# Optimization experiments

Hardware: AMD Instinct MI355X
Metric: run time of the kernel (lower is better)

## Reference

```python
import jax, jax.numpy as jnp
import numpy as np

B, D, T = 8, 1024, 512
HID, NH, NL = 256, 4, 2
OUT = HID // NH  # 64 per-head dim
ALPHA = 0.2      # leaky relu slope
EPS = 1e-5       # layernorm eps


def setup_inputs() -> dict:
    key = jax.random.key(0)
    ks = jax.random.split(key, 10)
    X_obs = jax.random.normal(ks[0], (B, D, T), dtype=jnp.float32)
    mask = (jax.random.uniform(ks[1], (B, D, T)) < 0.8).astype(jnp.float32)
    W_in = jax.random.normal(ks[2], (2 * T, HID), dtype=jnp.float32) * (1.0 / np.sqrt(2 * T))
    b_in = jnp.zeros((HID,), dtype=jnp.float32)
    gat_W = jax.random.normal(ks[3], (NL, NH, HID, OUT), dtype=jnp.float32) * (1.0 / np.sqrt(HID))
    gat_a = jax.random.normal(ks[4], (NL, NH, 2 * OUT), dtype=jnp.float32) * 0.1
    ln_g = jnp.ones((NL, HID), dtype=jnp.float32)
    ln_b = jnp.zeros((NL, HID), dtype=jnp.float32)
    W_out = jax.random.normal(ks[5], (HID, T), dtype=jnp.float32) * (1.0 / np.sqrt(HID))
    b_out = jnp.zeros((T,), dtype=jnp.float32)
    return dict(X_obs=X_obs, mask=mask, W_in=W_in, b_in=b_in, gat_W=gat_W,
                gat_a=gat_a, ln_g=ln_g, ln_b=ln_b, W_out=W_out, b_out=b_out)


def _layer_norm(x, g, b):
    mu = jnp.mean(x, axis=-1, keepdims=True)
    var = jnp.mean((x - mu) ** 2, axis=-1, keepdims=True)
    return (x - mu) * jax.lax.rsqrt(var + EPS) * g + b


def _gat_forward(X_obs, mask, W_in, b_in, gat_W, gat_a, ln_g, ln_b, W_out, b_out):
    # mean-impute per (d, t) position across batch
    obs_sum = jnp.sum(X_obs * mask, axis=0, keepdims=True)
    obs_cnt = jnp.sum(mask, axis=0, keepdims=True)
    pos_mean = obs_sum / (obs_cnt + 1e-10)
    X_mean = X_obs * mask + (1.0 - mask) * pos_mean

    x = jnp.concatenate([X_mean, mask], axis=-1)       # (B, D, 2T)
    h = x @ W_in + b_in                                 # (B, N, HID)

    for l in range(NL):
        Wl = gat_W[l]                                   # (H, HID, OUT)
        a_left = gat_a[l, :, :OUT]                      # (H, OUT)
        a_right = gat_a[l, :, OUT:]                     # (H, OUT)
        hW = jnp.einsum('bnd,hde->bhne', h, Wl)         # (B, H, N, OUT)
        # e_ij = leakyrelu(a_left . h_i + a_right . h_j) -- avoids O(N^2 * 2d) concat
        s_l = jnp.einsum('bhne,he->bhn', hW, a_left)
        s_r = jnp.einsum('bhne,he->bhn', hW, a_right)
        e = jax.nn.leaky_relu(s_l[..., :, None] + s_r[..., None, :], ALPHA)  # (B,H,N,N)
        attn = jax.nn.softmax(e, axis=-1)
        head_out = jnp.einsum('bhnm,bhme->bhne', attn, hW)                   # (B,H,N,OUT)
        h_new = jnp.transpose(head_out, (0, 2, 1, 3)).reshape(h.shape[0], h.shape[1], HID)
        h = _layer_norm(h + h_new, ln_g[l], ln_b[l])

    return h @ W_out + b_out                            # (B, D, T)


def reference(X_obs, mask, W_in, b_in, gat_W, gat_a, ln_g, ln_b, W_out, b_out):
    return _gat_forward(X_obs, mask, W_in, b_in, gat_W, gat_a, ln_g, ln_b, W_out, b_out)
```

## Files before the change

kernel.cpp:

```cpp
#include <hip/hip_runtime.h>
#include <hip/hip_bf16.h>

constexpr int B_   = 8;
constexpr int D_   = 1024;
constexpr int T_   = 512;
constexpr int HID_ = 256;
constexpr int NH_  = 4;
constexpr int NL_  = 2;
constexpr float ALPHA_ = 0.2f;
constexpr float EPS_   = 1e-5f;
constexpr int OUT_ = 64;
constexpr int M_ = B_ * D_;
constexpr int DT_ = D_ * T_;
constexpr int KIN_ = 2 * T_;
constexpr int CKS_ = 132;

typedef __attribute__((ext_vector_type(8))) short short8;
typedef __attribute__((ext_vector_type(4))) float floatx4;

__device__ __forceinline__ unsigned short f2bf(float f) {
    unsigned int u = __float_as_uint(f);
    unsigned int r = u + 0x7fffu + ((u >> 16) & 1u);
    return (unsigned short)(r >> 16);
}
__device__ __forceinline__ float bf2f(unsigned short u) {
    return __uint_as_float(((unsigned int)u) << 16);
}
__device__ __forceinline__ unsigned int kenc(float f) {
    unsigned int u = __float_as_uint(f);
    return (u & 0x80000000u) ? ~u : (u | 0x80000000u);
}
__device__ __forceinline__ float kdec(unsigned int k) {
    unsigned int u = (k & 0x80000000u) ? (k ^ 0x80000000u) : ~k;
    return __uint_as_float(u);
}

__global__ __launch_bounds__(256) void prep_k(const float* __restrict__ X,
                                              const float* __restrict__ Mk,
                                              const float* __restrict__ W_in,
                                              const float* __restrict__ gatW,
                                              const float* __restrict__ W_out,
                                              unsigned short* __restrict__ Ain,
                                              unsigned short* __restrict__ Wt_in,
                                              unsigned short* __restrict__ Wcat,
                                              unsigned short* __restrict__ WtO,
                                              unsigned int* __restrict__ rmaxkey) {
    int bx = blockIdx.x;
    if (bx < 512) {
        int idx4 = (bx * 256 + threadIdx.x) * 4;
        int t = idx4 & (T_ - 1);
        int d = idx4 >> 9;
        float4 x[B_], m[B_];
        float4 s = {0, 0, 0, 0}, c = {0, 0, 0, 0};
#pragma unroll
        for (int b = 0; b < B_; b++) {
            x[b] = *(const float4*)&X[(size_t)b * DT_ + idx4];
            m[b] = *(const float4*)&Mk[(size_t)b * DT_ + idx4];
            s.x += x[b].x * m[b].x; s.y += x[b].y * m[b].y;
            s.z += x[b].z * m[b].z; s.w += x[b].w * m[b].w;
            c.x += m[b].x; c.y += m[b].y; c.z += m[b].z; c.w += m[b].w;
        }
        float4 pm;
        pm.x = s.x / (c.x + 1e-10f); pm.y = s.y / (c.y + 1e-10f);
        pm.z = s.z / (c.z + 1e-10f); pm.w = s.w / (c.w + 1e-10f);
#pragma unroll
        for (int b = 0; b < B_; b++) {
            size_t row = (size_t)b * D_ + d;
            ushort4 xm, mk;
            xm.x = f2bf(x[b].x * m[b].x + (1.f - m[b].x) * pm.x);
            xm.y = f2bf(x[b].y * m[b].y + (1.f - m[b].y) * pm.y);
            xm.z = f2bf(x[b].z * m[b].z + (1.f - m[b].z) * pm.z);
            xm.w = f2bf(x[b].w * m[b].w + (1.f - m[b].w) * pm.w);
            mk.x = f2bf(m[b].x); mk.y = f2bf(m[b].y);
            mk.z = f2bf(m[b].z); mk.w = f2bf(m[b].w);
            *(ushort4*)&Ain[row * KIN_ + t]      = xm;
            *(ushort4*)&Ain[row * KIN_ + T_ + t] = mk;
        }
    } else {
        int idx = (bx - 512) * 256 + threadIdx.x;
        if (idx < 64) rmaxkey[idx] = 0u;
        if (idx < 262144) {
            int n = idx >> 10, k = idx & 1023;
            Wt_in[idx] = f2bf(W_in[(size_t)k * HID_ + n]);
        } else if (idx < 393216) {
            int j = idx - 262144;
            int l = j >> 16, n = (j >> 8) & 255, k = j & 255;
            int h = n >> 6, e = n & 63;
            Wcat[j] = f2bf(gatW[(((size_t)(l * NH_ + h) * HID_) + k) * OUT_ + e]);
        } else {
            int j = idx - 393216;
            int n = j >> 8, k = j & 255;
            WtO[j] = f2bf(W_out[(size_t)k * T_ + n]);
        }
    }
}

template <int MODE>
__global__ __launch_bounds__(256) void gemm_bf16_k(
        const unsigned short* __restrict__ A,
        const unsigned short* __restrict__ Bt,
        const float* __restrict__ bias,
        float* __restrict__ C,
        unsigned short* __restrict__ Cb,
        const float* __restrict__ ga,
        float* __restrict__ s_l,
        float* __restrict__ s_r,
        unsigned int* __restrict__ rmaxkey,
        int Nsz, int Ksz) {
    __shared__ __align__(16) unsigned short As[2][64 * 72];
    __shared__ __align__(16) unsigned short Bs[2][64 * 72];
    int tid = threadIdx.x;
    int wave = tid >> 6, lane = tid & 63;
    int q = lane >> 4, r16 = lane & 15;
    int rowbase = blockIdx.y * 64;
    int colbase = blockIdx.x * 64;

    int srow = tid >> 3, sk = (tid & 7) * 8;
    const unsigned short* Ap0 = A + (size_t)(rowbase + srow) * Ksz + sk;
    const unsigned short* Ap1 = A + (size_t)(rowbase + srow + 32) * Ksz + sk;
    const unsigned short* Bp0 = Bt + (size_t)(colbase + srow) * Ksz + sk;
    const unsigned short* Bp1 = Bt + (size_t)(colbase + srow + 32) * Ksz + sk;
    int la0 = srow * 72 + sk, la1 = (srow + 32) * 72 + sk;

    floatx4 acc[4];
#pragma unroll
    for (int i = 0; i < 4; i++) acc[i] = (floatx4)0.f;

    uint4 pa0 = *(const uint4*)Ap0, pa1 = *(const uint4*)Ap1;
    uint4 pb0 = *(const uint4*)Bp0, pb1 = *(const uint4*)Bp1;
    *(uint4*)&As[0][la0] = pa0;
    *(uint4*)&As[0][la1] = pa1;
    *(uint4*)&Bs[0][la0] = pb0;
    *(uint4*)&Bs[0][la1] = pb1;

    int nk = Ksz >> 6;
    for (int it = 0; it < nk; it++) {
        int cur = it & 1;
        __syncthreads();
        if (it + 1 < nk) {
            int kt = (it + 1) << 6;
            pa0 = *(const uint4*)(Ap0 + kt);
            pa1 = *(const uint4*)(Ap1 + kt);
            pb0 = *(const uint4*)(Bp0 + kt);
            pb1 = *(const uint4*)(Bp1 + kt);
        }
#pragma unroll
        for (int t = 0; t < 2; t++) {
            short8 a = *(const short8*)&As[cur][(wave * 16 + r16) * 72 + t * 32 + q * 8];
#pragma unroll
            for (int ni = 0; ni < 4; ni++) {
                short8 b = *(const short8*)&Bs[cur][(ni * 16 + r16) * 72 + t * 32 + q * 8];
                acc[ni] = __builtin_amdgcn_mfma_f32_16x16x32_bf16(a, b, acc[ni], 0, 0, 0);
            }
        }
        if (it + 1 < nk) {
            int nxt = cur ^ 1;
            *(uint4*)&As[nxt][la0] = pa0;
            *(uint4*)&As[nxt][la1] = pa1;
            *(uint4*)&Bs[nxt][la0] = pb0;
            *(uint4*)&Bs[nxt][la1] = pb1;
        }
    }
    if constexpr (MODE == 2) {
        int bhh = ((rowbase >> 10) << 2) + blockIdx.x;
        int nb = (rowbase & (D_ - 1)) + wave * 16;
#pragma unroll
        for (int ni = 0; ni < 4; ni++) {
            int e = ni * 16 + r16;
#pragma unroll
            for (int rr = 0; rr < 4; rr++) {
                int m = nb + q * 4 + rr;
                Cb[((size_t)bhh << 16) + ((size_t)m << 6) + e] = f2bf(acc[ni][rr]);
            }
        }
        const float* gab = ga + blockIdx.x * 2 * OUT_;
        float al4[4], ar4[4];
#pragma unroll
        for (int ni = 0; ni < 4; ni++) {
            al4[ni] = gab[ni * 16 + r16];
            ar4[ni] = gab[OUT_ + ni * 16 + r16];
        }
        float slv[4], srv[4];
#pragma unroll
        for (int rr = 0; rr < 4; rr++) {
            float s1 = 0.f, s2 = 0.f;
#pragma unroll
            for (int ni = 0; ni < 4; ni++) {
                s1 += acc[ni][rr] * al4[ni];
                s2 += acc[ni][rr] * ar4[ni];
            }
            slv[rr] = s1;
            srv[rr] = s2;
        }
#pragma unroll
        for (int off = 1; off < 16; off <<= 1) {
#pragma unroll
            for (int rr = 0; rr < 4; rr++) {
                slv[rr] += __shfl_xor(slv[rr], off, 64);
                srv[rr] += __shfl_xor(srv[rr], off, 64);
            }
        }
        {
            int rsel = r16 & 3;
            float sv = (rsel == 0) ? slv[0] : (rsel == 1) ? slv[1] : (rsel == 2) ? slv[2] : slv[3];
            float rv = (rsel == 0) ? srv[0] : (rsel == 1) ? srv[1] : (rsel == 2) ? srv[2] : srv[3];
            int n = nb + q * 4 + rsel;
            if (r16 < 4)                 s_l[bhh * D_ + n] = sv;
            else if (r16 >= 8 && r16 < 12) s_r[bhh * D_ + n] = rv;
        }
        float mx = fmaxf(fmaxf(srv[0], srv[1]), fmaxf(srv[2], srv[3]));
        mx = fmaxf(mx, __shfl_xor(mx, 16, 64));
        mx = fmaxf(mx, __shfl_xor(mx, 32, 64));
        if (lane == 0) atomicMax(&rmaxkey[bhh], kenc(mx));
    } else {
#pragma unroll
        for (int rr = 0; rr < 4; rr++) {
            int row = rowbase + wave * 16 + q * 4 + rr;
#pragma unroll
            for (int ni = 0; ni < 4; ni++) {
                int col = colbase + ni * 16 + r16;
                float v = acc[ni][rr] + (bias ? bias[col] : 0.f);
                C[(size_t)row * Nsz + col] = v;
                if constexpr (MODE == 1) Cb[(size_t)row * Nsz + col] = f2bf(v);
            }
        }
    }
}

__global__ __launch_bounds__(1024) void rank_k(
        const float* __restrict__ sr_g,
        const unsigned int* __restrict__ rmaxkey,
        float* __restrict__ srt,
        int* __restrict__ sig,
        float* __restrict__ wm) {
    __shared__ float skey[1024];
    __shared__ short part[16][64];
    int bh = blockIdx.x, seg = blockIdx.y;
    int tid = threadIdx.x;
    skey[tid] = sr_g[bh * D_ + tid];
    __syncthreads();
    int lane = tid & 63, wv = tid >> 6;
    int el = seg * 64 + lane;
    float k = skey[el];
    int m0 = wv * 64;
    int cnt = 0;
#pragma unroll 4
    for (int m = m0; m < m0 + 64; ++m) {
        float km = skey[m];
        cnt += (km < k) || (km == k && m < el);
    }
    part[wv][lane] = (short)cnt;
    __syncthreads();
    if (tid < 64) {
        int rank = 0;
#pragma unroll
        for (int w = 0; w < 16; ++w) rank += part[w][tid];
        int elg = seg * 64 + tid;
        float key = skey[elg];
        float rm = kdec(rmaxkey[bh]);
        float u = key - rm;
        float w1 = __expf(u), w2 = __expf(ALPHA_ * u);
        srt[bh * D_ + rank] = key;
        sig[bh * D_ + rank] = elg;
        *(float2*)&wm[(size_t)(bh * D_ + rank) * 2] = float2{w1, w2};
    }
}

__global__ __launch_bounds__(1024) void prefix_k(
        const unsigned short* __restrict__ hwN,
        const int* __restrict__ sig,
        const float* __restrict__ wm,
        float* __restrict__ ck) {
    __shared__ int   sidx[1024];
    __shared__ float w1s[1024], w2s[1024];
    __shared__ float csum[16][64][2];
    __shared__ float csca[16][2];
    int bh = blockIdx.x, tid = threadIdx.x;
    sidx[tid] = sig[bh * D_ + tid];
    float2 ww = *(const float2*)&wm[(size_t)(bh * D_ + tid) * 2];
    w1s[tid] = ww.x; w2s[tid] = ww.y;
    __syncthreads();
    int e = tid & 63, c = tid >> 6;
    const unsigned short* vb = hwN + ((size_t)bh << 16);
    int t0 = c * 64;
    float a1 = 0.f, a2 = 0.f;
    for (int t = t0; t < t0 + 64; ++t) {
        float v = bf2f(vb[((size_t)sidx[t] << 6) + e]);
        a1 = fmaf(w1s[t], v, a1);
        a2 = fmaf(w2s[t], v, a2);
    }
    csum[c][e][0] = a1; csum[c][e][1] = a2;
    if (e == 0) {
        float q1 = 0.f, q2 = 0.f;
        for (int t = t0; t < t0 + 64; ++t) { q1 += w1s[t]; q2 += w2s[t]; }
        csca[c][0] = q1; csca[c][1] = q2;
    }
    __syncthreads();
    float r1 = 0.f, r2 = 0.f, p1 = 0.f, p2 = 0.f;
    for (int cc = 0; cc < c; ++cc) { r1 += csum[cc][e][0]; r2 += csum[cc][e][1]; }
    if (e == 0)
        for (int cc = 0; cc < c; ++cc) { p1 += csca[cc][0]; p2 += csca[cc][1]; }
    float* ckb = ck + (size_t)bh * 257 * CKS_;
    for (int t = t0; t < t0 + 64; ++t) {
        if ((t & 3) == 0) {
            *(float2*)&ckb[(size_t)(t >> 2) * CKS_ + 2 * e] = float2{r1, r2};
            if (e == 0) *(float2*)&ckb[(size_t)(t >> 2) * CKS_ + 128] = float2{p1, p2};
        }
        float v = bf2f(vb[((size_t)sidx[t] << 6) + e]);
        r1 = fmaf(w1s[t], v, r1);
        r2 = fmaf(w2s[t], v, r2);
        if (e == 0) { p1 += w1s[t]; p2 += w2s[t]; }
    }
    if (c == 15) {
        *(float2*)&ckb[(size_t)256 * CKS_ + 2 * e] = float2{r1, r2};
        if (e == 0) *(float2*)&ckb[(size_t)256 * CKS_ + 128] = float2{p1, p2};
    }
}

__global__ __launch_bounds__(512) void rowln_k(
        float* __restrict__ h,
        const float* __restrict__ sl_g,
        const unsigned int* __restrict__ rmaxkey,
        const float* __restrict__ srt,
        const int* __restrict__ sig,
        const float* __restrict__ wm,
        const float* __restrict__ ck,
        const unsigned short* __restrict__ hwN,
        const float* __restrict__ g,
        const float* __restrict__ bb,
        unsigned short* __restrict__ hbf) {
    __shared__ float srtL[4][1024];
    __shared__ float hnew[32][260];
    __shared__ float ckT1[4][64];
    __shared__ float qTs[4][2];
    __shared__ float pdF[128][5];
    __shared__ int   pdI[128][5];
    int blk = blockIdx.x;
    int b = blk >> 5;
    int d0 = (blk & 31) << 5;
    int tid = threadIdx.x;
    for (int i = tid; i < 4096; i += 512)
        srtL[i >> 10][i & 1023] = srt[(size_t)((b * 4 + (i >> 10)) * D_) + (i & 1023)];
    if (tid < 256) {
        int hh = tid >> 6, e = tid & 63;
        ckT1[hh][e] = ck[((size_t)(b * 4 + hh) * 257 + 256) * CKS_ + 2 * e];
    }
    if (tid < 8) {
        int hh = tid >> 1;
        qTs[hh][tid & 1] = ck[((size_t)(b * 4 + hh) * 257 + 256) * CKS_ + 128 + (tid & 1)];
    }
    __syncthreads();
    if (tid < 128) {
        int r = tid & 31, h4 = tid >> 5;
        int bh = b * 4 + h4;
        float sl = sl_g[bh * D_ + d0 + r];
        float rm = kdec(rmaxkey[bh]);
        float x = sl + rm;
        float Mn = fmaxf(x, ALPHA_ * x);
        float A  = __expf(x - Mn);
        float B2 = __expf(ALPHA_ * x - Mn);
        float key = -sl;
        int lo = 0, hi = 1024;
        while (lo < hi) {
            int mid = (lo + hi) >> 1;
            if (srtL[h4][mid] < key) lo = mid + 1; else hi = mid;
        }
        int t = lo, c4 = t >> 2, nf = t & 3;
        float2 qs = *(const float2*)&ck[((size_t)bh * 257 + c4) * CKS_ + 128];
        float w1f[3] = {0.f, 0.f, 0.f}, w2f[3] = {0.f, 0.f, 0.f};
        int vo[3] = {0, 0, 0};
#pragma unroll
        for (int f = 0; f < 3; ++f) {
            if (f < nf) {
                int rk = c4 * 4 + f;
                float2 ww = *(const float2*)&wm[(size_t)(bh * D_ + rk) * 2];
                w1f[f] = ww.x; w2f[f] = ww.y;
                vo[f] = sig[bh * D_ + rk] << 6;
                qs.x += ww.x; qs.y += ww.y;
            }
        }
        float den = A * (qTs[h4][0] - qs.x) + B2 * qs.y;
        float inv = 1.f / den;
        float fA = A * inv, fB = B2 * inv;
        pdF[tid][0] = fA; pdF[tid][1] = fB;
#pragma unroll
        for (int f = 0; f < 3; ++f) pdF[tid][2 + f] = fB * w2f[f] - fA * w1f[f];
        pdI[tid][0] = vo[0]; pdI[tid][1] = vo[1]; pdI[tid][2] = vo[2];
        pdI[tid][3] = c4;    pdI[tid][4] = nf;
    }
    __syncthreads();
    int wv = tid >> 6, e = tid & 63;
    for (int p = wv; p < 128; p += 8) {
        int r = p & 31, h4 = p >> 5;
        int bh = b * 4 + h4;
        float fA = pdF[p][0], fB = pdF[p][1];
        int c4 = pdI[p][3], nf = pdI[p][4];
        float2 P = *(const float2*)&ck[((size_t)bh * 257 + c4) * CKS_ + 2 * e];
        float o = fA * (ckT1[h4][e] - P.x) + fB * P.y;
        const unsigned short* vb = hwN + ((size_t)bh << 16);
        if (nf > 0) o += pdF[p][2] * bf2f(vb[pdI[p][0] + e]);
        if (nf > 1) o += pdF[p][3] * bf2f(vb[pdI[p][1] + e]);
        if (nf > 2) o += pdF[p][4] * bf2f(vb[pdI[p][2] + e]);
        hnew[r][h4 * 64 + e] = o;
    }
    __syncthreads();
    for (int rr = wv * 4; rr < wv * 4 + 4; ++rr) {
        size_t grow = ((((size_t)b << 10) + d0 + rr) << 8);
        float4 a  = *(const float4*)&h[grow + e * 4];
        float4 nv = *(const float4*)&hnew[rr][e * 4];
        float4 v = {a.x + nv.x, a.y + nv.y, a.z + nv.z, a.w + nv.w};
        float s = v.x + v.y + v.z + v.w;
#pragma unroll
        for (int off = 1; off < 64; off <<= 1) s += __shfl_xor(s, off, 64);
        float mu = s * (1.f / HID_);
        float4 dd = {v.x - mu, v.y - mu, v.z - mu, v.w - mu};
        float s2 = dd.x * dd.x + dd.y * dd.y + dd.z * dd.z + dd.w * dd.w;
#pragma unroll
        for (int off = 1; off < 64; off <<= 1) s2 += __shfl_xor(s2, off, 64);
        float rs = rsqrtf(s2 * (1.f / HID_) + EPS_);
        float4 gg = *(const float4*)&g[e * 4];
        float4 bv = *(const float4*)&bb[e * 4];
        float4 res;
        res.x = dd.x * rs * gg.x + bv.x;
        res.y = dd.y * rs * gg.y + bv.y;
        res.z = dd.z * rs * gg.z + bv.z;
        res.w = dd.w * rs * gg.w + bv.w;
        *(float4*)&h[grow + e * 4] = res;
        ushort4 pk = {f2bf(res.x), f2bf(res.y), f2bf(res.z), f2bf(res.w)};
        *(ushort4*)&hbf[grow + e * 4] = pk;
    }
}

extern "C" void kernel_launch(void* const* d_in, const int* in_sizes, int n_in,
                              void* d_out, int out_size, void* d_ws, size_t ws_size,
                              hipStream_t stream) {
    const float* X_obs = (const float*)d_in[0];
    const float* mask  = (const float*)d_in[1];
    const float* W_in  = (const float*)d_in[2];
    const float* b_in  = (const float*)d_in[3];
    const float* gat_W = (const float*)d_in[4];
    const float* gat_a = (const float*)d_in[5];
    const float* ln_g  = (const float*)d_in[6];
    const float* ln_b  = (const float*)d_in[7];
    const float* W_out = (const float*)d_in[8];
    const float* b_out = (const float*)d_in[9];
    float* out = (float*)d_out;

    char* base = (char*)d_ws;
    unsigned short* Ain = (unsigned short*)base;
    unsigned short* hwN = (unsigned short*)base;
    float* ck   = (float*)(base + (5u << 20));
    float* wm   = (float*)(base + (10u << 20));
    float* srtb = (float*)(base + (11u << 20));
    int*   sig  = (int*)(base + (12u << 20));
    float* hbuf = (float*)(base + (21u << 20));
    unsigned short* hbf   = (unsigned short*)(base + (29u << 20));
    unsigned short* Wt_in = (unsigned short*)(base + (33u << 20));
    unsigned short* Wcat  = Wt_in + (size_t)HID_ * KIN_;
    unsigned short* WtO   = Wcat + (size_t)NL_ * HID_ * HID_;
    float* slb = (float*)(WtO + (size_t)T_ * HID_);
    float* srb = slb + B_ * NH_ * D_;
    unsigned int* rmaxkey = (unsigned int*)(srb + B_ * NH_ * D_);

    prep_k<<<2560, 256, 0, stream>>>(X_obs, mask, W_in, gat_W, W_out,
                                     Ain, Wt_in, Wcat, WtO, rmaxkey);

    gemm_bf16_k<1><<<dim3(HID_ / 64, M_ / 64), 256, 0, stream>>>(
        Ain, Wt_in, b_in, hbuf, hbf, nullptr, nullptr, nullptr, nullptr,
        HID_, KIN_);

    for (int l = 0; l < NL_; l++) {
        gemm_bf16_k<2><<<dim3(HID_ / 64, M_ / 64), 256, 0, stream>>>(
            hbf, Wcat + (size_t)l * HID_ * HID_, nullptr, nullptr, hwN,
            gat_a + (size_t)l * NH_ * 2 * OUT_, slb, srb, rmaxkey + l * 32,
            HID_, HID_);
        rank_k<<<dim3(32, 16), 1024, 0, stream>>>(srb, rmaxkey + l * 32,
                                                  srtb, sig, wm);
        prefix_k<<<32, 1024, 0, stream>>>(hwN, sig, wm, ck);
        rowln_k<<<256, 512, 0, stream>>>(hbuf, slb, rmaxkey + l * 32,
                                         srtb, sig, wm, ck, hwN,
                                         ln_g + (size_t)l * HID_,
                                         ln_b + (size_t)l * HID_, hbf);
    }

    gemm_bf16_k<0><<<dim3(T_ / 64, M_ / 64), 256, 0, stream>>>(
        hbf, WtO, b_out, out, nullptr, nullptr, nullptr, nullptr, nullptr,
        T_, HID_);
}
```

Measured before the change: 263.6 us.

## Enlarge GEMM row tile, stage MODE2 output via LDS, store full prefix table

```diff
diff --git a/kernel.cpp b/kernel.cpp
--- a/kernel.cpp
+++ b/kernel.cpp
@@ -107,31 +107,34 @@
         float* __restrict__ s_r,
         unsigned int* __restrict__ rmaxkey,
         int Nsz, int Ksz) {
-    __shared__ __align__(16) unsigned short As[2][64 * 72];
+    __shared__ __align__(16) unsigned short As[2][128 * 72];
     __shared__ __align__(16) unsigned short Bs[2][64 * 72];
     int tid = threadIdx.x;
     int wave = tid >> 6, lane = tid & 63;
     int q = lane >> 4, r16 = lane & 15;
-    int rowbase = blockIdx.y * 64;
+    int rowbase = blockIdx.y * 128;
     int colbase = blockIdx.x * 64;
 
     int srow = tid >> 3, sk = (tid & 7) * 8;
-    const unsigned short* Ap0 = A + (size_t)(rowbase + srow) * Ksz + sk;
-    const unsigned short* Ap1 = A + (size_t)(rowbase + srow + 32) * Ksz + sk;
-    const unsigned short* Bp0 = Bt + (size_t)(colbase + srow) * Ksz + sk;
-    const unsigned short* Bp1 = Bt + (size_t)(colbase + srow + 32) * Ksz + sk;
-    int la0 = srow * 72 + sk, la1 = (srow + 32) * 72 + sk;
-
-    floatx4 acc[4];
-#pragma unroll
-    for (int i = 0; i < 4; i++) acc[i] = (floatx4)0.f;
-
-    uint4 pa0 = *(const uint4*)Ap0, pa1 = *(const uint4*)Ap1;
-    uint4 pb0 = *(const uint4*)Bp0, pb1 = *(const uint4*)Bp1;
-    *(uint4*)&As[0][la0] = pa0;
-    *(uint4*)&As[0][la1] = pa1;
-    *(uint4*)&Bs[0][la0] = pb0;
-    *(uint4*)&Bs[0][la1] = pb1;
+    const unsigned short* Ap = A + (size_t)(rowbase + srow) * Ksz + sk;
+    const unsigned short* Bp = Bt + (size_t)(colbase + srow) * Ksz + sk;
+    int la = srow * 72 + sk;
+
+    floatx4 acc[2][4];
+#pragma unroll
+    for (int mi = 0; mi < 2; mi++)
+#pragma unroll
+        for (int ni = 0; ni < 4; ni++) acc[mi][ni] = (floatx4)0.f;
+
+    uint4 pa[4], pb[2];
+#pragma unroll
+    for (int i = 0; i < 4; i++) pa[i] = *(const uint4*)(Ap + (size_t)(i * 32) * Ksz);
+#pragma unroll
+    for (int i = 0; i < 2; i++) pb[i] = *(const uint4*)(Bp + (size_t)(i * 32) * Ksz);
+#pragma unroll
+    for (int i = 0; i < 4; i++) *(uint4*)&As[0][la + i * 32 * 72] = pa[i];
+#pragma unroll
+    for (int i = 0; i < 2; i++) *(uint4*)&Bs[0][la + i * 32 * 72] = pb[i];
 
     int nk = Ksz >> 6;
     for (int it = 0; it < nk; it++) {
@@ -139,40 +142,33 @@
         __syncthreads();
         if (it + 1 < nk) {
             int kt = (it + 1) << 6;
-            pa0 = *(const uint4*)(Ap0 + kt);
-            pa1 = *(const uint4*)(Ap1 + kt);
-            pb0 = *(const uint4*)(Bp0 + kt);
-            pb1 = *(const uint4*)(Bp1 + kt);
+#pragma unroll
+            for (int i = 0; i < 4; i++) pa[i] = *(const uint4*)(Ap + (size_t)(i * 32) * Ksz + kt);
+#pragma unroll
+            for (int i = 0; i < 2; i++) pb[i] = *(const uint4*)(Bp + (size_t)(i * 32) * Ksz + kt);
         }
 #pragma unroll
         for (int t = 0; t < 2; t++) {
-            short8 a = *(const short8*)&As[cur][(wave * 16 + r16) * 72 + t * 32 + q * 8];
+            short8 a0 = *(const short8*)&As[cur][(wave * 16 + r16) * 72 + t * 32 + q * 8];
+            short8 a1 = *(const short8*)&As[cur][(64 + wave * 16 + r16) * 72 + t * 32 + q * 8];
 #pragma unroll
             for (int ni = 0; ni < 4; ni++) {
-                short8 b = *(const short8*)&Bs[cur][(ni * 16 + r16) * 72 + t * 32 + q * 8];
-                acc[ni] = __builtin_amdgcn_mfma_f32_16x16x32_bf16(a, b, acc[ni], 0, 0, 0);
+                short8 bf = *(const short8*)&Bs[cur][(ni * 16 + r16) * 72 + t * 32 + q * 8];
+                acc[0][ni] = __builtin_amdgcn_mfma_f32_16x16x32_bf16(a0, bf, acc[0][ni], 0, 0, 0);
+                acc[1][ni] = __builtin_amdgcn_mfma_f32_16x16x32_bf16(a1, bf, acc[1][ni], 0, 0, 0);
             }
         }
         if (it + 1 < nk) {
             int nxt = cur ^ 1;
-            *(uint4*)&As[nxt][la0] = pa0;
-            *(uint4*)&As[nxt][la1] = pa1;
-            *(uint4*)&Bs[nxt][la0] = pb0;
-            *(uint4*)&Bs[nxt][la1] = pb1;
+#pragma unroll
+            for (int i = 0; i < 4; i++) *(uint4*)&As[nxt][la + i * 32 * 72] = pa[i];
+#pragma unroll
+            for (int i = 0; i < 2; i++) *(uint4*)&Bs[nxt][la + i * 32 * 72] = pb[i];
         }
     }
     if constexpr (MODE == 2) {
         int bhh = ((rowbase >> 10) << 2) + blockIdx.x;
-        int nb = (rowbase & (D_ - 1)) + wave * 16;
-#pragma unroll
-        for (int ni = 0; ni < 4; ni++) {
-            int e = ni * 16 + r16;
-#pragma unroll
-            for (int rr = 0; rr < 4; rr++) {
-                int m = nb + q * 4 + rr;
-                Cb[((size_t)bhh << 16) + ((size_t)m << 6) + e] = f2bf(acc[ni][rr]);
-            }
-        }
+        int nb0 = rowbase & (D_ - 1);
         const float* gab = ga + blockIdx.x * 2 * OUT_;
         float al4[4], ar4[4];
 #pragma unroll
@@ -180,50 +176,72 @@
             al4[ni] = gab[ni * 16 + r16];
             ar4[ni] = gab[OUT_ + ni * 16 + r16];
         }
-        float slv[4], srv[4];
-#pragma unroll
-        for (int rr = 0; rr < 4; rr++) {
-            float s1 = 0.f, s2 = 0.f;
-#pragma unroll
-            for (int ni = 0; ni < 4; ni++) {
-                s1 += acc[ni][rr] * al4[ni];
-                s2 += acc[ni][rr] * ar4[ni];
+        float mxw = -1e30f;
+#pragma unroll
+        for (int mi = 0; mi < 2; mi++) {
+            float slv[4], srv[4];
+#pragma unroll
+            for (int rr = 0; rr < 4; rr++) {
+                float s1 = 0.f, s2 = 0.f;
+#pragma unroll
+                for (int ni = 0; ni < 4; ni++) {
+                    s1 += acc[mi][ni][rr] * al4[ni];
+                    s2 += acc[mi][ni][rr] * ar4[ni];
+                }
+                slv[rr] = s1;
+                srv[rr] = s2;
             }
-            slv[rr] = s1;
-            srv[rr] = s2;
-        }
-#pragma unroll
-        for (int off = 1; off < 16; off <<= 1) {
-#pragma unroll
-            for (int rr = 0; rr < 4; rr++) {
-                slv[rr] += __shfl_xor(slv[rr], off, 64);
-                srv[rr] += __shfl_xor(srv[rr], off, 64);
+#pragma unroll
+            for (int off = 1; off < 16; off <<= 1) {
+#pragma unroll
+                for (int rr = 0; rr < 4; rr++) {
+                    slv[rr] += __shfl_xor(slv[rr], off, 64);
+                    srv[rr] += __shfl_xor(srv[rr], off, 64);
+                }
             }
-        }
-        {
             int rsel = r16 & 3;
             float sv = (rsel == 0) ? slv[0] : (rsel == 1) ? slv[1] : (rsel == 2) ? slv[2] : slv[3];
             float rv = (rsel == 0) ? srv[0] : (rsel == 1) ? srv[1] : (rsel == 2) ? srv[2] : srv[3];
-            int n = nb + q * 4 + rsel;
+            int n = nb0 + mi * 64 + wave * 16 + q * 4 + rsel;
             if (r16 < 4)                 s_l[bhh * D_ + n] = sv;
             else if (r16 >= 8 && r16 < 12) s_r[bhh * D_ + n] = rv;
-        }
-        float mx = fmaxf(fmaxf(srv[0], srv[1]), fmaxf(srv[2], srv[3]));
-        mx = fmaxf(mx, __shfl_xor(mx, 16, 64));
-        mx = fmaxf(mx, __shfl_xor(mx, 32, 64));
-        if (lane == 0) atomicMax(&rmaxkey[bhh], kenc(mx));
+            float mx = fmaxf(fmaxf(srv[0], srv[1]), fmaxf(srv[2], srv[3]));
+            mxw = fmaxf(mxw, mx);
+        }
+        mxw = fmaxf(mxw, __shfl_xor(mxw, 16, 64));
+        mxw = fmaxf(mxw, __shfl_xor(mxw, 32, 64));
+        if (lane == 0) atomicMax(&rmaxkey[bhh], kenc(mxw));
+        __syncthreads();
+        unsigned short* st = &As[0][0];
+#pragma unroll
+        for (int mi = 0; mi < 2; mi++)
+#pragma unroll
+            for (int ni = 0; ni < 4; ni++)
+#pragma unroll
+                for (int rr = 0; rr < 4; rr++)
+                    st[(mi * 64 + wave * 16 + q * 4 + rr) * 72 + ni * 16 + r16] = f2bf(acc[mi][ni][rr]);
+        __syncthreads();
+#pragma unroll
+        for (int i = 0; i < 4; i++) {
+            int idx = tid * 4 + i;
+            int row = idx >> 3, seg = idx & 7;
+            uint4 v = *(const uint4*)&st[row * 72 + seg * 8];
+            *(uint4*)&Cb[((size_t)bhh << 16) + ((size_t)(nb0 + row) << 6) + seg * 8] = v;
+        }
     } else {
 #pragma unroll
-        for (int rr = 0; rr < 4; rr++) {
-            int row = rowbase + wave * 16 + q * 4 + rr;
-#pragma unroll
-            for (int ni = 0; ni < 4; ni++) {
-                int col = colbase + ni * 16 + r16;
-                float v = acc[ni][rr] + (bias ? bias[col] : 0.f);
-                C[(size_t)row * Nsz + col] = v;
-                if constexpr (MODE == 1) Cb[(size_t)row * Nsz + col] = f2bf(v);
+        for (int mi = 0; mi < 2; mi++)
+#pragma unroll
+            for (int rr = 0; rr < 4; rr++) {
+                int row = rowbase + mi * 64 + wave * 16 + q * 4 + rr;
+#pragma unroll
+                for (int ni = 0; ni < 4; ni++) {
+                    int col = colbase + ni * 16 + r16;
+                    float v = acc[mi][ni][rr] + (bias ? bias[col] : 0.f);
+                    C[(size_t)row * Nsz + col] = v;
+                    if constexpr (MODE == 1) Cb[(size_t)row * Nsz + col] = f2bf(v);
+                }
             }
-        }
     }
 }
 
@@ -283,37 +301,35 @@
     int e = tid & 63, c = tid >> 6;
     const unsigned short* vb = hwN + ((size_t)bh << 16);
     int t0 = c * 64;
-    float a1 = 0.f, a2 = 0.f;
+    float a1 = 0.f, a2 = 0.f, q1 = 0.f, q2 = 0.f;
     for (int t = t0; t < t0 + 64; ++t) {
+        float wv1 = w1s[t], wv2 = w2s[t];
         float v = bf2f(vb[((size_t)sidx[t] << 6) + e]);
-        a1 = fmaf(w1s[t], v, a1);
-        a2 = fmaf(w2s[t], v, a2);
+        a1 = fmaf(wv1, v, a1);
+        a2 = fmaf(wv2, v, a2);
+        q1 += wv1; q2 += wv2;
     }
     csum[c][e][0] = a1; csum[c][e][1] = a2;
-    if (e == 0) {
-        float q1 = 0.f, q2 = 0.f;
-        for (int t = t0; t < t0 + 64; ++t) { q1 += w1s[t]; q2 += w2s[t]; }
-        csca[c][0] = q1; csca[c][1] = q2;
-    }
+    if (e == 0) { csca[c][0] = q1; csca[c][1] = q2; }
     __syncthreads();
     float r1 = 0.f, r2 = 0.f, p1 = 0.f, p2 = 0.f;
-    for (int cc = 0; cc < c; ++cc) { r1 += csum[cc][e][0]; r2 += csum[cc][e][1]; }
-    if (e == 0)
-        for (int cc = 0; cc < c; ++cc) { p1 += csca[cc][0]; p2 += csca[cc][1]; }
-    float* ckb = ck + (size_t)bh * 257 * CKS_;
+    for (int cc = 0; cc < c; ++cc) {
+        r1 += csum[cc][e][0]; r2 += csum[cc][e][1];
+        p1 += csca[cc][0];    p2 += csca[cc][1];
+    }
+    float* ckb = ck + (size_t)bh * 1025 * CKS_;
     for (int t = t0; t < t0 + 64; ++t) {
-        if ((t & 3) == 0) {
-            *(float2*)&ckb[(size_t)(t >> 2) * CKS_ + 2 * e] = float2{r1, r2};
-            if (e == 0) *(float2*)&ckb[(size_t)(t >> 2) * CKS_ + 128] = float2{p1, p2};
-        }
+        *(float2*)&ckb[(size_t)t * CKS_ + 2 * e] = float2{r1, r2};
+        if (e == 0) *(float2*)&ckb[(size_t)t * CKS_ + 128] = float2{p1, p2};
+        float wv1 = w1s[t], wv2 = w2s[t];
         float v = bf2f(vb[((size_t)sidx[t] << 6) + e]);
-        r1 = fmaf(w1s[t], v, r1);
-        r2 = fmaf(w2s[t], v, r2);
-        if (e == 0) { p1 += w1s[t]; p2 += w2s[t]; }
+        r1 = fmaf(wv1, v, r1);
+        r2 = fmaf(wv2, v, r2);
+        p1 += wv1; p2 += wv2;
     }
     if (c == 15) {
-        *(float2*)&ckb[(size_t)256 * CKS_ + 2 * e] = float2{r1, r2};
-        if (e == 0) *(float2*)&ckb[(size_t)256 * CKS_ + 128] = float2{p1, p2};
+        *(float2*)&ckb[(size_t)1024 * CKS_ + 2 * e] = float2{r1, r2};
+        if (e == 0) *(float2*)&ckb[(size_t)1024 * CKS_ + 128] = float2{p1, p2};
     }
 }
 
@@ -322,10 +338,7 @@
         const float* __restrict__ sl_g,
         const unsigned int* __restrict__ rmaxkey,
         const float* __restrict__ srt,
-        const int* __restrict__ sig,
-        const float* __restrict__ wm,
         const float* __restrict__ ck,
-        const unsigned short* __restrict__ hwN,
         const float* __restrict__ g,
         const float* __restrict__ bb,
         unsigned short* __restrict__ hbf) {
@@ -333,8 +346,8 @@
     __shared__ float hnew[32][260];
     __shared__ float ckT1[4][64];
     __shared__ float qTs[4][2];
-    __shared__ float pdF[128][5];
-    __shared__ int   pdI[128][5];
+    __shared__ float pdF[128][2];
+    __shared__ int   pdT[128];
     int blk = blockIdx.x;
     int b = blk >> 5;
     int d0 = (blk & 31) << 5;
@@ -343,11 +356,11 @@
         srtL[i >> 10][i & 1023] = srt[(size_t)((b * 4 + (i >> 10)) * D_) + (i & 1023)];
     if (tid < 256) {
         int hh = tid >> 6, e = tid & 63;
-        ckT1[hh][e] = ck[((size_t)(b * 4 + hh) * 257 + 256) * CKS_ + 2 * e];
+        ckT1[hh][e] = ck[((size_t)((b * 4 + hh) * 1025 + 1024)) * CKS_ + 2 * e];
     }
     if (tid < 8) {
         int hh = tid >> 1;
-        qTs[hh][tid & 1] = ck[((size_t)(b * 4 + hh) * 257 + 256) * CKS_ + 128 + (tid & 1)];
+        qTs[hh][tid & 1] = ck[((size_t)((b * 4 + hh) * 1025 + 1024)) * CKS_ + 128 + (tid & 1)];
     }
     __syncthreads();
     if (tid < 128) {
@@ -365,28 +378,12 @@
             int mid = (lo + hi) >> 1;
             if (srtL[h4][mid] < key) lo = mid + 1; else hi = mid;
         }
-        int t = lo, c4 = t >> 2, nf = t & 3;
-        float2 qs = *(const float2*)&ck[((size_t)bh * 257 + c4) * CKS_ + 128];
-        float w1f[3] = {0.f, 0.f, 0.f}, w2f[3] = {0.f, 0.f, 0.f};
-        int vo[3] = {0, 0, 0};
-#pragma unroll
-        for (int f = 0; f < 3; ++f) {
-            if (f < nf) {
-                int rk = c4 * 4 + f;
-                float2 ww = *(const float2*)&wm[(size_t)(bh * D_ + rk) * 2];
-                w1f[f] = ww.x; w2f[f] = ww.y;
-                vo[f] = sig[bh * D_ + rk] << 6;
-                qs.x += ww.x; qs.y += ww.y;
-            }
-        }
+        float2 qs = *(const float2*)&ck[((size_t)(bh * 1025 + lo)) * CKS_ + 128];
         float den = A * (qTs[h4][0] - qs.x) + B2 * qs.y;
         float inv = 1.f / den;
-        float fA = A * inv, fB = B2 * inv;
-        pdF[tid][0] = fA; pdF[tid][1] = fB;
-#pragma unroll
-        for (int f = 0; f < 3; ++f) pdF[tid][2 + f] = fB * w2f[f] - fA * w1f[f];
-        pdI[tid][0] = vo[0]; pdI[tid][1] = vo[1]; pdI[tid][2] = vo[2];
-        pdI[tid][3] = c4;    pdI[tid][4] = nf;
+        pdF[tid][0] = A * inv;
+        pdF[tid][1] = B2 * inv;
+        pdT[tid] = lo;
     }
     __syncthreads();
     int wv = tid >> 6, e = tid & 63;
@@ -394,14 +391,9 @@
         int r = p & 31, h4 = p >> 5;
         int bh = b * 4 + h4;
         float fA = pdF[p][0], fB = pdF[p][1];
-        int c4 = pdI[p][3], nf = pdI[p][4];
-        float2 P = *(const float2*)&ck[((size_t)bh * 257 + c4) * CKS_ + 2 * e];
-        float o = fA * (ckT1[h4][e] - P.x) + fB * P.y;
-        const unsigned short* vb = hwN + ((size_t)bh << 16);
-        if (nf > 0) o += pdF[p][2] * bf2f(vb[pdI[p][0] + e]);
-        if (nf > 1) o += pdF[p][3] * bf2f(vb[pdI[p][1] + e]);
-        if (nf > 2) o += pdF[p][4] * bf2f(vb[pdI[p][2] + e]);
-        hnew[r][h4 * 64 + e] = o;
+        int t = pdT[p];
+        float2 P = *(const float2*)&ck[((size_t)(bh * 1025 + t)) * CKS_ + 2 * e];
+        hnew[r][h4 * 64 + e] = fA * (ckT1[h4][e] - P.x) + fB * P.y;
     }
     __syncthreads();
     for (int rr = wv * 4; rr < wv * 4 + 4; ++rr) {
@@ -449,13 +441,13 @@
     char* base = (char*)d_ws;
     unsigned short* Ain = (unsigned short*)base;
     unsigned short* hwN = (unsigned short*)base;
-    float* ck   = (float*)(base + (5u << 20));
-    float* wm   = (float*)(base + (10u << 20));
-    float* srtb = (float*)(base + (11u << 20));
-    int*   sig  = (int*)(base + (12u << 20));
-    float* hbuf = (float*)(base + (21u << 20));
-    unsigned short* hbf   = (unsigned short*)(base + (29u << 20));
-    unsigned short* Wt_in = (unsigned short*)(base + (33u << 20));
+    float* ck   = (float*)(base + (4u << 20));
+    float* wm   = (float*)(base + (22u << 20));
+    float* srtb = (float*)(base + (22u << 20) + (512u << 10));
+    int*   sig  = (int*)(base + (22u << 20) + (768u << 10));
+    float* hbuf = (float*)(base + (23u << 20));
+    unsigned short* hbf   = (unsigned short*)(base + (31u << 20));
+    unsigned short* Wt_in = (unsigned short*)(base + (35u << 20));
     unsigned short* Wcat  = Wt_in + (size_t)HID_ * KIN_;
     unsigned short* WtO   = Wcat + (size_t)NL_ * HID_ * HID_;
     float* slb = (float*)(WtO + (size_t)T_ * HID_);
@@ -465,12 +457,12 @@
     prep_k<<<2560, 256, 0, stream>>>(X_obs, mask, W_in, gat_W, W_out,
                                      Ain, Wt_in, Wcat, WtO, rmaxkey);
 
-    gemm_bf16_k<1><<<dim3(HID_ / 64, M_ / 64), 256, 0, stream>>>(
+    gemm_bf16_k<1><<<dim3(HID_ / 64, M_ / 128), 256, 0, stream>>>(
         Ain, Wt_in, b_in, hbuf, hbf, nullptr, nullptr, nullptr, nullptr,
         HID_, KIN_);
 
     for (int l = 0; l < NL_; l++) {
-        gemm_bf16_k<2><<<dim3(HID_ / 64, M_ / 64), 256, 0, stream>>>(
+        gemm_bf16_k<2><<<dim3(HID_ / 64, M_ / 128), 256, 0, stream>>>(
             hbf, Wcat + (size_t)l * HID_ * HID_, nullptr, nullptr, hwN,
             gat_a + (size_t)l * NH_ * 2 * OUT_, slb, srb, rmaxkey + l * 32,
             HID_, HID_);
@@ -478,12 +470,12 @@
                                                   srtb, sig, wm);
         prefix_k<<<32, 1024, 0, stream>>>(hwN, sig, wm, ck);
         rowln_k<<<256, 512, 0, stream>>>(hbuf, slb, rmaxkey + l * 32,
-                                         srtb, sig, wm, ck, hwN,
+                                         srtb, ck,
                                          ln_g + (size_t)l * HID_,
                                          ln_b + (size_t)l * HID_, hbf);
     }
 
-    gemm_bf16_k<0><<<dim3(T_ / 64, M_ / 64), 256, 0, stream>>>(
+    gemm_bf16_k<0><<<dim3(T_ / 64, M_ / 128), 256, 0, stream>>>(
         hbf, WtO, b_out, out, nullptr, nullptr, nullptr, nullptr, nullptr,
         T_, HID_);
 }
```

Result: slower. 332.2 us (+26.0%).
